# Kernel optimization log

Hardware: AMD Instinct MI355X
Metric: run time of the kernel (lower is better)

## Reference

```python
import jax, jax.numpy as jnp
import numpy as np

HIDDEN = 1024
B, S = 4, 2048

def setup_inputs() -> dict:
    key = jax.random.key(0)
    k1, k2 = jax.random.split(key)
    hidden_states = jax.random.normal(k1, (B, S, HIDDEN), dtype=jnp.float32)
    # torch nn.Linear weight layout: [out_features, in_features]
    W_proj = jax.random.normal(k2, (3 * HIDDEN, HIDDEN), dtype=jnp.float32) * (1.0 / np.sqrt(HIDDEN))
    b_proj = jnp.zeros((3 * HIDDEN,), dtype=jnp.float32)
    return {"hidden_states": hidden_states, "W_proj": W_proj, "b_proj": b_proj}

def reference(hidden_states, W_proj, b_proj):
    h = hidden_states.shape[-1]
    # fused QKV projection: y = x @ W^T + b
    qkv = jnp.einsum('bsh,oh->bso', hidden_states, W_proj) + b_proj
    q, k, v = jnp.split(qkv, 3, axis=-1)  # each [B,S,H]
    scale = 1.0 / jnp.sqrt(jnp.asarray(h, dtype=q.dtype))
    scores = jnp.einsum('bqh,bkh->bqk', q, k) * scale  # [B,S,S]
    attn = jax.nn.softmax(scores, axis=-1)
    out = jnp.einsum('bqk,bkh->bqh', attn, v)
    return out
```

## Files before the change

### kernel.cpp

```cpp
#include <hip/hip_runtime.h>
#include <stdint.h>

#define HIDDEN 1024
#define BATCH  4
#define SEQ    2048
#define TOKENS (BATCH * SEQ)
#define QKVD   (3 * HIDDEN)

typedef unsigned short u16;
typedef __attribute__((ext_vector_type(8))) short   short8;
typedef __attribute__((ext_vector_type(4))) float   floatx4;

__device__ __forceinline__ u16 f32_bf16_rne(float f) {
    unsigned int u = __float_as_uint(f);
    u += 0x7FFFu + ((u >> 16) & 1u);
    return (u16)(u >> 16);
}

__global__ __launch_bounds__(256) void cvt_bf16_kernel(
        const float* __restrict__ src, u16* __restrict__ dst, int n4) {
    int i = blockIdx.x * 256 + threadIdx.x;
    if (i >= n4) return;
    float4 v = ((const float4*)src)[i];
    ushort4 o;
    o.x = f32_bf16_rne(v.x); o.y = f32_bf16_rne(v.y);
    o.z = f32_bf16_rne(v.z); o.w = f32_bf16_rne(v.w);
    ((ushort4*)dst)[i] = o;
}

template <int EPI>
__global__ __launch_bounds__(256) void gemm_bt(
        const u16* __restrict__ A, const u16* __restrict__ B,
        void* __restrict__ Cv, const float* __restrict__ bias,
        int K, int lda, int ldb, int ldc,
        size_t sA, size_t sB, size_t sC, float scale) {
    __shared__ u16 As[2][128 * 32];
    __shared__ u16 Bs[2][128 * 32];

    const int t    = threadIdx.x;
    const int lane = t & 63;
    const int wid  = t >> 6;
    const int bm   = blockIdx.y * 128;
    const int bn   = blockIdx.x * 128;

    const u16* Ab = A + (size_t)blockIdx.z * sA;
    const u16* Bb = B + (size_t)blockIdx.z * sB;

    const int srow = lane >> 2;
    const int scol = ((lane & 3) ^ ((lane >> 3) & 3)) * 8;

    const int wm = (wid >> 1) * 64;
    const int wn = (wid & 1) * 64;
    const int fr = lane & 15;
    const int fc = lane >> 4;
    const int foff = fr * 32 + ((fc ^ ((fr >> 1) & 3)) * 8);

    const int c0 = wid * 2, c1 = wid * 2 + 1;
    const u16* gA0 = Ab + (size_t)(bm + c0 * 16 + srow) * lda + scol;
    const u16* gA1 = Ab + (size_t)(bm + c1 * 16 + srow) * lda + scol;
    const u16* gB0 = Bb + (size_t)(bn + c0 * 16 + srow) * ldb + scol;
    const u16* gB1 = Bb + (size_t)(bn + c1 * 16 + srow) * ldb + scol;

    auto stage = [&](int buf, int k0) {
        __builtin_amdgcn_global_load_lds(
            (const __attribute__((address_space(1))) void*)(gA0 + k0),
            (__attribute__((address_space(3))) void*)(&As[buf][c0 * 512]), 16, 0, 0);
        __builtin_amdgcn_global_load_lds(
            (const __attribute__((address_space(1))) void*)(gB0 + k0),
            (__attribute__((address_space(3))) void*)(&Bs[buf][c0 * 512]), 16, 0, 0);
        __builtin_amdgcn_global_load_lds(
            (const __attribute__((address_space(1))) void*)(gA1 + k0),
            (__attribute__((address_space(3))) void*)(&As[buf][c1 * 512]), 16, 0, 0);
        __builtin_amdgcn_global_load_lds(
            (const __attribute__((address_space(1))) void*)(gB1 + k0),
            (__attribute__((address_space(3))) void*)(&Bs[buf][c1 * 512]), 16, 0, 0);
    };

    floatx4 acc[4][4];
#pragma unroll
    for (int i = 0; i < 4; i++)
#pragma unroll
        for (int j = 0; j < 4; j++) acc[i][j] = (floatx4){0.f, 0.f, 0.f, 0.f};

    stage(0, 0);

    int cur = 0;
    for (int k0 = 0; k0 < K; k0 += 32) {
        __syncthreads();
        if (k0 + 32 < K) stage(cur ^ 1, k0 + 32);

        short8 af[4], bf[4];
#pragma unroll
        for (int mi = 0; mi < 4; mi++)
            af[mi] = *(const short8*)&As[cur][((wm >> 4) + mi) * 512 + foff];
#pragma unroll
        for (int ni = 0; ni < 4; ni++)
            bf[ni] = *(const short8*)&Bs[cur][((wn >> 4) + ni) * 512 + foff];
#pragma unroll
        for (int mi = 0; mi < 4; mi++)
#pragma unroll
            for (int ni = 0; ni < 4; ni++)
                acc[mi][ni] = __builtin_amdgcn_mfma_f32_16x16x32_bf16(
                    af[mi], bf[ni], acc[mi][ni], 0, 0, 0);
        cur ^= 1;
    }

    const int crow0 = bm + wm + (lane >> 4) * 4;
    const int ccol0 = bn + wn + fr;
    const size_t coff = (size_t)blockIdx.z * sC;

    if (EPI == 0) {
        u16* C = (u16*)Cv;
        float bv[4];
#pragma unroll
        for (int ni = 0; ni < 4; ni++) bv[ni] = bias[ccol0 + ni * 16];
#pragma unroll
        for (int mi = 0; mi < 4; mi++)
#pragma unroll
            for (int ni = 0; ni < 4; ni++)
#pragma unroll
                for (int r = 0; r < 4; r++)
                    C[coff + (size_t)(crow0 + mi * 16 + r) * ldc + (ccol0 + ni * 16)] =
                        f32_bf16_rne(acc[mi][ni][r] + bv[ni]);
    } else {
        float* C = (float*)Cv;
#pragma unroll
        for (int mi = 0; mi < 4; mi++)
#pragma unroll
            for (int ni = 0; ni < 4; ni++)
#pragma unroll
                for (int r = 0; r < 4; r++) {
                    float v = acc[mi][ni][r];
                    if (EPI == 1) v *= scale;
                    C[coff + (size_t)(crow0 + mi * 16 + r) * ldc + (ccol0 + ni * 16)] = v;
                }
    }
}

__global__ __launch_bounds__(256) void softmax_kernel(
        const float* __restrict__ S, u16* __restrict__ P) {
    __shared__ float redm[4];
    __shared__ float reds[4];
    const size_t base = (size_t)blockIdx.x * SEQ;
    const int t = threadIdx.x, lane = t & 63, wid = t >> 6;
    const float4* src = (const float4*)(S + base);
    float4 a = src[t], b = src[t + 256];

    float m = fmaxf(fmaxf(fmaxf(a.x, a.y), fmaxf(a.z, a.w)),
                    fmaxf(fmaxf(b.x, b.y), fmaxf(b.z, b.w)));
#pragma unroll
    for (int off = 32; off; off >>= 1) m = fmaxf(m, __shfl_xor(m, off, 64));
    if (lane == 0) redm[wid] = m;
    __syncthreads();
    m = fmaxf(fmaxf(redm[0], redm[1]), fmaxf(redm[2], redm[3]));

    float e[8];
    e[0] = __expf(a.x - m); e[1] = __expf(a.y - m);
    e[2] = __expf(a.z - m); e[3] = __expf(a.w - m);
    e[4] = __expf(b.x - m); e[5] = __expf(b.y - m);
    e[6] = __expf(b.z - m); e[7] = __expf(b.w - m);
    float s = e[0] + e[1] + e[2] + e[3] + e[4] + e[5] + e[6] + e[7];
#pragma unroll
    for (int off = 32; off; off >>= 1) s += __shfl_xor(s, off, 64);
    if (lane == 0) reds[wid] = s;
    __syncthreads();
    s = reds[0] + reds[1] + reds[2] + reds[3];
    const float r = 1.f / s;

    ushort4* dst = (ushort4*)(P + base);
    ushort4 o0, o1;
    o0.x = f32_bf16_rne(e[0] * r); o0.y = f32_bf16_rne(e[1] * r);
    o0.z = f32_bf16_rne(e[2] * r); o0.w = f32_bf16_rne(e[3] * r);
    o1.x = f32_bf16_rne(e[4] * r); o1.y = f32_bf16_rne(e[5] * r);
    o1.z = f32_bf16_rne(e[6] * r); o1.w = f32_bf16_rne(e[7] * r);
    dst[t] = o0;
    dst[t + 256] = o1;
}

__global__ __launch_bounds__(256) void transposeV_kernel(
        const u16* __restrict__ qkv, u16* __restrict__ Vt) {
    __shared__ u16 tile[64][66];
    const int b = blockIdx.z;
    const int s0 = blockIdx.x * 64, h0 = blockIdx.y * 64;
    const int t = threadIdx.x;
    const int c = t & 63, r4 = t >> 6;
#pragma unroll
    for (int i = 0; i < 16; i++) {
        int sl = i * 4 + r4;
        tile[sl][c] = qkv[(size_t)(b * SEQ + s0 + sl) * QKVD + 2 * HIDDEN + h0 + c];
    }
    __syncthreads();
#pragma unroll
    for (int i = 0; i < 16; i++) {
        int hl = i * 4 + r4;
        Vt[(size_t)(b * HIDDEN + h0 + hl) * SEQ + s0 + c] = tile[c][hl];
    }
}

extern "C" void kernel_launch(void* const* d_in, const int* in_sizes, int n_in,
                              void* d_out, int out_size, void* d_ws, size_t ws_size,
                              hipStream_t stream) {
    const float* x    = (const float*)d_in[0];
    const float* W    = (const float*)d_in[1];
    const float* bias = (const float*)d_in[2];
    float* out = (float*)d_out;

    u16* Xb  = (u16*)d_ws;
    u16* Wb  = Xb + (size_t)TOKENS * HIDDEN;
    u16* qkv = Wb + (size_t)QKVD * HIDDEN;
    float* scores = (float*)(qkv + (size_t)TOKENS * QKVD);
    u16* P  = (u16*)(scores + (size_t)BATCH * SEQ * SEQ);
    u16* Vt = P + (size_t)BATCH * SEQ * SEQ;

    cvt_bf16_kernel<<<TOKENS * HIDDEN / 4 / 256, 256, 0, stream>>>(x, Xb, TOKENS * HIDDEN / 4);
    cvt_bf16_kernel<<<QKVD * HIDDEN / 4 / 256, 256, 0, stream>>>(W, Wb, QKVD * HIDDEN / 4);

    gemm_bt<0><<<dim3(QKVD / 128, TOKENS / 128, 1), 256, 0, stream>>>(
        Xb, Wb, qkv, bias, HIDDEN, HIDDEN, HIDDEN, QKVD, 0, 0, 0, 1.f);

    gemm_bt<1><<<dim3(SEQ / 128, SEQ / 128, BATCH), 256, 0, stream>>>(
        qkv, qkv + HIDDEN, scores, nullptr, HIDDEN, QKVD, QKVD, SEQ,
        (size_t)SEQ * QKVD, (size_t)SEQ * QKVD, (size_t)SEQ * SEQ, 0.03125f);

    softmax_kernel<<<BATCH * SEQ, 256, 0, stream>>>(scores, P);

    transposeV_kernel<<<dim3(SEQ / 64, HIDDEN / 64, BATCH), 256, 0, stream>>>(qkv, Vt);

    gemm_bt<2><<<dim3(HIDDEN / 128, SEQ / 128, BATCH), 256, 0, stream>>>(
        P, Vt, out, nullptr, SEQ, SEQ, SEQ, HIDDEN,
        (size_t)SEQ * SEQ, (size_t)HIDDEN * SEQ, (size_t)SEQ * HIDDEN, 1.f);
}
```

Measured before the change: 291.8 us.

## Replace direct-to-LDS loads with register-staged two-tile prefetch pipeline in GEMM

Changes the shared GEMM main loop from direct global-to-LDS loads to loads into registers, fetched two K-tiles ahead and then written to a ping-pong pair of LDS buffers. Each tile needs only one `s_waitcnt lgkmcnt(0)` plus barrier. The aim is to hide global memory latency behind the MFMA work and to cut barrier overhead. The A fragments are now loaded one at a time inside the MFMA loop. Launch bounds ask for 3 blocks per SM, which may limit registers. The extra registers held by the staged tiles could cause spills or lower occupancy.

New measurement: 275.3 us. -5.6%, faster.

```diff
diff --git a/kernel.cpp b/kernel.cpp
--- a/kernel.cpp
+++ b/kernel.cpp
@@ -16,6 +16,8 @@
     u += 0x7FFFu + ((u >> 16) & 1u);
     return (u16)(u >> 16);
 }
+
+#define BAR() asm volatile("s_waitcnt lgkmcnt(0)\n\ts_barrier" ::: "memory")
 
 __global__ __launch_bounds__(256) void cvt_bf16_kernel(
         const float* __restrict__ src, u16* __restrict__ dst, int n4) {
@@ -28,14 +30,16 @@
     ((ushort4*)dst)[i] = o;
 }
 
+struct Stage { uint4 a0, a1, b0, b1; };
+
 template <int EPI>
-__global__ __launch_bounds__(256) void gemm_bt(
+__global__ __launch_bounds__(256, 3) void gemm_bt(
         const u16* __restrict__ A, const u16* __restrict__ B,
         void* __restrict__ Cv, const float* __restrict__ bias,
         int K, int lda, int ldb, int ldc,
         size_t sA, size_t sB, size_t sC, float scale) {
-    __shared__ u16 As[2][128 * 32];
-    __shared__ u16 Bs[2][128 * 32];
+    __shared__ u16 As0[4096], As1[4096];
+    __shared__ u16 Bs0[4096], Bs1[4096];
 
     const int t    = threadIdx.x;
     const int lane = t & 63;
@@ -61,20 +65,23 @@
     const u16* gB0 = Bb + (size_t)(bn + c0 * 16 + srow) * ldb + scol;
     const u16* gB1 = Bb + (size_t)(bn + c1 * 16 + srow) * ldb + scol;
 
-    auto stage = [&](int buf, int k0) {
-        __builtin_amdgcn_global_load_lds(
-            (const __attribute__((address_space(1))) void*)(gA0 + k0),
-            (__attribute__((address_space(3))) void*)(&As[buf][c0 * 512]), 16, 0, 0);
-        __builtin_amdgcn_global_load_lds(
-            (const __attribute__((address_space(1))) void*)(gB0 + k0),
-            (__attribute__((address_space(3))) void*)(&Bs[buf][c0 * 512]), 16, 0, 0);
-        __builtin_amdgcn_global_load_lds(
-            (const __attribute__((address_space(1))) void*)(gA1 + k0),
-            (__attribute__((address_space(3))) void*)(&As[buf][c1 * 512]), 16, 0, 0);
-        __builtin_amdgcn_global_load_lds(
-            (const __attribute__((address_space(1))) void*)(gB1 + k0),
-            (__attribute__((address_space(3))) void*)(&Bs[buf][c1 * 512]), 16, 0, 0);
+    const int nk = K >> 5;
+
+    auto ldst = [&](int kt) -> Stage {
+        Stage s;
+        const int off = kt << 5;
+        s.a0 = *(const uint4*)(gA0 + off);
+        s.a1 = *(const uint4*)(gA1 + off);
+        s.b0 = *(const uint4*)(gB0 + off);
+        s.b1 = *(const uint4*)(gB1 + off);
+        return s;
     };
+    auto wst = [&](u16* As_, u16* Bs_, const Stage& s) {
+        *(uint4*)&As_[c0 * 512 + lane * 8] = s.a0;
+        *(uint4*)&As_[c1 * 512 + lane * 8] = s.a1;
+        *(uint4*)&Bs_[c0 * 512 + lane * 8] = s.b0;
+        *(uint4*)&Bs_[c1 * 512 + lane * 8] = s.b1;
+    };
 
     floatx4 acc[4][4];
 #pragma unroll
@@ -82,27 +89,35 @@
 #pragma unroll
         for (int j = 0; j < 4; j++) acc[i][j] = (floatx4){0.f, 0.f, 0.f, 0.f};
 
-    stage(0, 0);
-
-    int cur = 0;
-    for (int k0 = 0; k0 < K; k0 += 32) {
-        __syncthreads();
-        if (k0 + 32 < K) stage(cur ^ 1, k0 + 32);
-
-        short8 af[4], bf[4];
-#pragma unroll
-        for (int mi = 0; mi < 4; mi++)
-            af[mi] = *(const short8*)&As[cur][((wm >> 4) + mi) * 512 + foff];
+    auto compute = [&](const u16* As_, const u16* Bs_) {
+        short8 bfr[4];
 #pragma unroll
         for (int ni = 0; ni < 4; ni++)
-            bf[ni] = *(const short8*)&Bs[cur][((wn >> 4) + ni) * 512 + foff];
-#pragma unroll
-        for (int mi = 0; mi < 4; mi++)
+            bfr[ni] = *(const short8*)&Bs_[((wn >> 4) + ni) * 512 + foff];
+#pragma unroll
+        for (int mi = 0; mi < 4; mi++) {
+            short8 a = *(const short8*)&As_[((wm >> 4) + mi) * 512 + foff];
 #pragma unroll
             for (int ni = 0; ni < 4; ni++)
                 acc[mi][ni] = __builtin_amdgcn_mfma_f32_16x16x32_bf16(
-                    af[mi], bf[ni], acc[mi][ni], 0, 0, 0);
-        cur ^= 1;
+                    a, bfr[ni], acc[mi][ni], 0, 0, 0);
+        }
+    };
+
+    Stage ra = ldst(0);
+    Stage rb = ldst(nk > 1 ? 1 : 0);
+    wst(As0, Bs0, ra);
+    BAR();
+
+    for (int kt = 0; kt < nk; kt += 2) {
+        ra = ldst(kt + 2 < nk ? kt + 2 : nk - 1);
+        compute(As0, Bs0);
+        wst(As1, Bs1, rb);
+        BAR();
+        rb = ldst(kt + 3 < nk ? kt + 3 : nk - 1);
+        compute(As1, Bs1);
+        wst(As0, Bs0, ra);
+        BAR();
     }
 
     const int crow0 = bm + wm + (lane >> 4) * 4;
```
